# Kernel optimization log

Hardware: AMD Instinct MI355X
Metric: run time of the kernel (lower is better)

The kernel has to match this reference:

```python
import jax, jax.numpy as jnp
import numpy as np

B, V, T = 512, 50257, 2048   # batch, vocab, history length
TOP_K = 50                    # from __init__ arg top_k
NEG_INF = jnp.float32(-1e30)  # finite stand-in for -inf (same softmax result, clean grads)


def setup_inputs() -> dict:
    key = jax.random.key(0)
    k1, k2, k3 = jax.random.split(key, 3)
    logits = jax.random.normal(k1, (B, V), jnp.float32) * 4.0
    previous_tokens = jax.random.randint(k2, (B, T), 0, V)
    # uniform noise for the Gumbel-max trick (torch.rand_like); avoid log(0)
    rand_u = jax.random.uniform(k3, (B, V), jnp.float32, minval=1e-10, maxval=1.0)
    return {
        "logits": logits,
        "previous_tokens": previous_tokens,
        "rand_u": rand_u,
        "temperature": jnp.full((1, 1), 0.8, jnp.float32),
        "top_p": jnp.full((1, 1), 0.8, jnp.float32),
        "repetition_penalty": jnp.full((1, 1), 1.35, jnp.float32),
    }


def _logits_to_probs(logits, previous_tokens, temperature, top_p, repetition_penalty):
    b = jnp.arange(logits.shape[0])[:, None]
    # repetition penalty: gather scores at previous tokens, rescale, scatter back
    score = jnp.take_along_axis(logits, previous_tokens, axis=1)            # [B, T]
    score = jnp.where(score < 0, score * repetition_penalty, score / repetition_penalty)
    logits = logits.at[b, previous_tokens].set(score)
    # top-p (nucleus) filtering: sort descending, cumulative softmax mass
    order = jnp.argsort(-logits, axis=-1)                                   # [B, V]
    sorted_logits = jnp.take_along_axis(logits, order, axis=1)
    cum_probs = jnp.cumsum(jax.nn.softmax(sorted_logits, axis=-1), axis=-1)
    remove_sorted = cum_probs > top_p
    remove_sorted = remove_sorted.at[:, 0].set(False)                       # always keep best token
    # unsort the removal mask back to vocab order (order is a permutation)
    remove = jnp.zeros_like(remove_sorted).at[b, order].set(remove_sorted)
    logits = jnp.where(remove, NEG_INF, logits)
    # temperature
    logits = logits / jnp.maximum(temperature, 1e-5)
    # top-k filtering: mask everything below the k-th largest logit
    v = jax.lax.top_k(logits, TOP_K)[0]                                     # [B, TOP_K]
    pivot = v[:, -1:]
    logits = jnp.where(logits < pivot, NEG_INF, logits)
    return jax.nn.softmax(logits, axis=-1)


def reference(logits, previous_tokens, rand_u, temperature, top_p, repetition_penalty):
    probs = _logits_to_probs(logits, previous_tokens, temperature, top_p, repetition_penalty)
    # Gumbel-max multinomial sample: argmax(probs / Exp(1))
    q = -jnp.log(rand_u)
    idx_next = jnp.argmax(probs / q, axis=-1, keepdims=True).astype(jnp.int64)
    return idx_next, probs
```

## Files before the change

### kernel.cpp

```cpp
#include <hip/hip_runtime.h>
#include <cstdint>
#include <cmath>

#define V_SIZE 50257
#define T_SIZE 2048
#define B_SIZE 512
#define NTHR 1024
#define NWAVE (NTHR / 64)
#define CAND_MAX 1024
#define SPEC_THRESH 10.0f
#define SPEC_MIN 80
#define KOFF 32.0f

extern "C" __global__ __launch_bounds__(NTHR, 8)
void decode_kernel(const float* __restrict__ logits,
                   const int*   __restrict__ prev,
                   const float* __restrict__ rand_u,
                   const float* __restrict__ tempp,
                   const float* __restrict__ toppp,
                   const float* __restrict__ repp,
                   float* __restrict__ out)
{
    const int row  = blockIdx.x;
    const int tid  = threadIdx.x;
    const int lane = tid & 63;
    const int wid  = tid >> 6;

    __shared__ unsigned int bitmap[(V_SIZE + 31) / 32];
    __shared__ float cval[CAND_MAX];
    __shared__ int   cidx[CAND_MAX];
    __shared__ float rbuf[CAND_MAX];
    __shared__ float redf[NWAVE];
    __shared__ int   redi[NWAVE];
    __shared__ float sM, sZ, sS;
    __shared__ int   sCnt, sSend;

    const float rp   = repp[0];
    const float topp = toppp[0];
    const float temp = fmaxf(tempp[0], 1e-5f);

    const size_t rowoff = (size_t)row * V_SIZE;
    const float* lrow = logits + rowoff;
    const float* urow = rand_u + rowoff;
    float*       orow = out + B_SIZE + rowoff;

    for (int i = tid; i < (V_SIZE + 31) / 32; i += NTHR) bitmap[i] = 0u;
    if (tid == 0) sCnt = 0;
    __syncthreads();

    const int4* prow4 = (const int4*)(prev + (size_t)row * T_SIZE);
    for (int i = tid; i < T_SIZE / 4; i += NTHR) {
        int4 t = prow4[i];
        atomicOr(&bitmap[((unsigned)t.x) >> 5], 1u << (t.x & 31));
        atomicOr(&bitmap[((unsigned)t.y) >> 5], 1u << (t.y & 31));
        atomicOr(&bitmap[((unsigned)t.z) >> 5], 1u << (t.z & 31));
        atomicOr(&bitmap[((unsigned)t.w) >> 5], 1u << (t.w & 31));
    }
    __syncthreads();

    const int head  = (4 - (row & 3)) & 3;
    const int nvec  = (V_SIZE - head) >> 2;
    const int tails = head + nvec * 4;
    const float4* lrow4 = (const float4*)(lrow + head);

    float lm = -INFINITY, lz = 0.0f;
    auto process1 = [&](float x, int v) {
        unsigned w = bitmap[v >> 5];
        if ((w >> (v & 31)) & 1u) x = (x < 0.0f) ? x * rp : x / rp;
        if (x > SPEC_THRESH) {
            int p = atomicAdd(&sCnt, 1);
            if (p < CAND_MAX) { cval[p] = x; cidx[p] = v; }
        }
        lm = fmaxf(lm, x);
        lz += __expf(x - KOFF);
    };
    if (tid < head)           process1(lrow[tid], tid);
    if (tid < V_SIZE - tails) process1(lrow[tails + tid], tails + tid);
    for (int i = tid; i < nvec; i += NTHR) {
        float4 x4 = lrow4[i];
        int v = head + i * 4;
        process1(x4.x, v); process1(x4.y, v + 1);
        process1(x4.z, v + 2); process1(x4.w, v + 3);
    }

    {
        float wm = lm;
        for (int off = 32; off; off >>= 1) wm = fmaxf(wm, __shfl_down(wm, off));
        if (lane == 0) redf[wid] = wm;
    }
    __syncthreads();
    if (tid == 0) {
        float m = redf[0];
        for (int i = 1; i < NWAVE; ++i) m = fmaxf(m, redf[i]);
        sM = m;
    }
    __syncthreads();
    const float M = sM;

    {
        float wz = lz;
        for (int off = 32; off; off >>= 1) wz += __shfl_down(wz, off);
        if (lane == 0) redf[wid] = wz;
    }
    __syncthreads();
    if (tid == 0) {
        float s = 0.0f;
        for (int i = 0; i < NWAVE; ++i) s += redf[i];
        sZ = s * expf(KOFF - M);
    }
    __syncthreads();
    const float Z = sZ;

    int cnt = sCnt;
    int C;
    if (cnt >= SPEC_MIN && cnt <= CAND_MAX) {
        C = cnt;
    } else {
        auto count_pass = [&](float thr) -> int {
            __syncthreads();
            if (tid == 0) sCnt = 0;
            __syncthreads();
            int local = 0;
            for (int v = tid; v < V_SIZE; v += NTHR) {
                float x = lrow[v];
                unsigned w = bitmap[v >> 5];
                if ((w >> (v & 31)) & 1u) x = (x < 0.0f) ? x * rp : x / rp;
                if (x > thr) local++;
            }
            if (local) atomicAdd(&sCnt, local);
            __syncthreads();
            return sCnt;
        };
        float a = -200.0f, b = 200.0f, thr = 0.0f;
        int c = 0;
        for (int it = 0; it < 40; ++it) {
            thr = 0.5f * (a + b);
            c = count_pass(thr);
            if (c < SPEC_MIN)       b = thr;
            else if (c > CAND_MAX)  a = thr;
            else break;
        }
        if (c < SPEC_MIN) thr = a;
        __syncthreads();
        if (tid == 0) sCnt = 0;
        __syncthreads();
        for (int v = tid; v < V_SIZE; v += NTHR) {
            float x = lrow[v];
            unsigned w = bitmap[v >> 5];
            if ((w >> (v & 31)) & 1u) x = (x < 0.0f) ? x * rp : x / rp;
            if (x > thr) {
                int p = atomicAdd(&sCnt, 1);
                if (p < CAND_MAX) { cval[p] = x; cidx[p] = v; }
            }
        }
        __syncthreads();
        C = min(sCnt, CAND_MAX);
    }

    int n = 1; while (n < C) n <<= 1;
    for (int i = C + tid; i < n; i += NTHR) { cval[i] = -INFINITY; cidx[i] = 0x7FFFFFFF; }
    __syncthreads();
    for (int k = 2; k <= n; k <<= 1) {
        for (int j = k >> 1; j > 0; j >>= 1) {
            for (int i = tid; i < n; i += NTHR) {
                int l = i ^ j;
                if (l > i) {
                    float vi = cval[i], vl = cval[l];
                    int   ii = cidx[i], il = cidx[l];
                    bool lFirst = (vl > vi) || (vl == vi && il < ii);
                    bool asc = ((i & k) == 0);
                    if (lFirst == asc) {
                        cval[i] = vl; cval[l] = vi;
                        cidx[i] = il; cidx[l] = ii;
                    }
                }
            }
            __syncthreads();
        }
    }

    if (tid == 0) {
        float cum = 0.0f;
        int m = 0;
        float vp = cval[min(49, C - 1)];
        for (int i = 0; i < C; ++i) {
            cum += expf(cval[i] - M) / Z;
            if (i > 0 && cum > topp) break;
            m = i;
            if (m >= 49 && cval[i] < vp) break;
        }
        int send;
        if (m >= 49) {
            int e = 49;
            while (e + 1 < C && cval[e + 1] == vp) ++e;
            send = (m < e) ? m : e;
        } else {
            send = m;
        }
        sSend = send;
    }
    __syncthreads();

    const int send = sSend;
    const float v0 = cval[0];
    for (int i = tid; i <= send; i += NTHR)
        rbuf[i] = expf(cval[i] / temp - v0 / temp);
    __syncthreads();
    if (tid == 0) {
        float S = 0.0f;
        for (int i = 0; i <= send; ++i) S += rbuf[i];
        sS = S;
    }
    __syncthreads();
    const float S = sS;

    float bestr = -1.0f;
    int   besti = 0x7FFFFFFF;
    for (int i = tid; i <= send; i += NTHR) {
        float p = rbuf[i] / S;
        int v = cidx[i];
        orow[v] = p;
        float q = -logf(urow[v]);
        float r = p / q;
        if (r > bestr || (r == bestr && v < besti)) { bestr = r; besti = v; }
    }
    for (int off = 32; off; off >>= 1) {
        float r2 = __shfl_down(bestr, off);
        int   i2 = __shfl_down(besti, off);
        if (r2 > bestr || (r2 == bestr && i2 < besti)) { bestr = r2; besti = i2; }
    }
    if (lane == 0) { redf[wid] = bestr; redi[wid] = besti; }
    __syncthreads();
    if (tid == 0) {
        float br = redf[0]; int bi = redi[0];
        for (int i = 1; i < NWAVE; ++i) {
            if (redf[i] > br || (redf[i] == br && redi[i] < bi)) { br = redf[i]; bi = redi[i]; }
        }
        out[row] = (float)bi;
    }
}

extern "C" void kernel_launch(void* const* d_in, const int* in_sizes, int n_in,
                              void* d_out, int out_size, void* d_ws, size_t ws_size,
                              hipStream_t stream) {
    const float* logits = (const float*)d_in[0];
    const int*   prev   = (const int*)d_in[1];
    const float* rand_u = (const float*)d_in[2];
    const float* tempp  = (const float*)d_in[3];
    const float* toppp  = (const float*)d_in[4];
    const float* repp   = (const float*)d_in[5];
    float* out = (float*)d_out;

    hipMemsetAsync(d_out, 0, (size_t)out_size * sizeof(float), stream);

    hipLaunchKernelGGL(decode_kernel, dim3(B_SIZE), dim3(NTHR), 0, stream,
                       logits, prev, rand_u, tempp, toppp, repp, out);
}
```

Measured before the change: 261.5 us.

## Split row processing into chunked streaming kernel plus per-row tail kernel

Splits the single per-row kernel into two. The first launches 8 chunks per row, computing a partial softmax normaliser with a fixed offset and collecting high-logit candidates into a global workspace through atomics. The second applies the repetition penalty as a sparse correction to the normaliser and candidate values, then sorts the candidates and samples. This spreads the full-vocab streaming pass across more blocks and removes the bitmap lookup and max reduction from the hot loop, at the cost of an extra launch, a workspace memset and global atomics. It also relies on the fixed offset not overflowing and adds a fallback condition for when the penalty changes the candidate set.

```diff
diff --git a/kernel.cpp b/kernel.cpp
--- a/kernel.cpp
+++ b/kernel.cpp
@@ -5,21 +5,77 @@
 #define V_SIZE 50257
 #define T_SIZE 2048
 #define B_SIZE 512
-#define NTHR 1024
-#define NWAVE (NTHR / 64)
-#define CAND_MAX 1024
+#define CHUNKS 8
+#define CHUNK_LEN ((V_SIZE + CHUNKS - 1) / CHUNKS)
+#define NTHR_A 256
+#define NTHR_B 512
+#define NWAVE_B (NTHR_B / 64)
+#define CAP 512
 #define SPEC_THRESH 10.0f
 #define SPEC_MIN 80
 #define KOFF 32.0f
 
-extern "C" __global__ __launch_bounds__(NTHR, 8)
-void decode_kernel(const float* __restrict__ logits,
-                   const int*   __restrict__ prev,
-                   const float* __restrict__ rand_u,
-                   const float* __restrict__ tempp,
-                   const float* __restrict__ toppp,
-                   const float* __restrict__ repp,
-                   float* __restrict__ out)
+
+extern "C" __global__ __launch_bounds__(NTHR_A, 8)
+void stream_kernel(const float* __restrict__ logits,
+                   float* __restrict__ gZ, int* __restrict__ gcnt,
+                   float* __restrict__ gval, int* __restrict__ gidx)
+{
+    const int row = blockIdx.y;
+    const int tid = threadIdx.x;
+    const size_t rowoff = (size_t)row * V_SIZE;
+    const float* lrow = logits + rowoff;
+    const int lo = blockIdx.x * CHUNK_LEN;
+    const int hi = min(V_SIZE, lo + CHUNK_LEN);
+
+    float lz = 0.0f;
+    auto proc = [&](float x, int v) {
+        lz += __expf(x - KOFF);
+        if (x > SPEC_THRESH) {
+            int p = atomicAdd(&gcnt[row], 1);
+            if (p < CAP) {
+                gval[(size_t)row * CAP + p] = x;
+                gidx[(size_t)row * CAP + p] = v;
+            }
+        }
+    };
+
+    int a0 = lo + (int)((4u - ((unsigned)(rowoff + lo) & 3u)) & 3u);
+    if (a0 > hi) a0 = hi;
+    const int nv = (hi - a0) >> 2;
+    const int t0 = a0 + nv * 4;
+    if (tid < a0 - lo) proc(lrow[lo + tid], lo + tid);
+    if (tid < hi - t0) proc(lrow[t0 + tid], t0 + tid);
+    const float4* l4 = (const float4*)(lrow + a0);
+    for (int i = tid; i < nv; i += NTHR_A) {
+        float4 x4 = l4[i];
+        int v = a0 + i * 4;
+        proc(x4.x, v); proc(x4.y, v + 1); proc(x4.z, v + 2); proc(x4.w, v + 3);
+    }
+
+    __shared__ float red[NTHR_A / 64];
+    for (int off = 32; off; off >>= 1) lz += __shfl_down(lz, off);
+    if ((tid & 63) == 0) red[tid >> 6] = lz;
+    __syncthreads();
+    if (tid == 0) {
+        float s = 0.0f;
+        for (int i = 0; i < NTHR_A / 64; ++i) s += red[i];
+        atomicAdd(&gZ[row], s);
+    }
+}
+
+extern "C" __global__ __launch_bounds__(NTHR_B, 4)
+void tail_kernel(const float* __restrict__ logits,
+                 const int*   __restrict__ prev,
+                 const float* __restrict__ rand_u,
+                 const float* __restrict__ tempp,
+                 const float* __restrict__ toppp,
+                 const float* __restrict__ repp,
+                 const float* __restrict__ gZ,
+                 const int*   __restrict__ gcnt,
+                 const float* __restrict__ gval,
+                 const int*   __restrict__ gidx,
+                 float* __restrict__ out)
 {
     const int row  = blockIdx.x;
     const int tid  = threadIdx.x;
@@ -27,13 +83,13 @@
     const int wid  = tid >> 6;
 
     __shared__ unsigned int bitmap[(V_SIZE + 31) / 32];
-    __shared__ float cval[CAND_MAX];
-    __shared__ int   cidx[CAND_MAX];
-    __shared__ float rbuf[CAND_MAX];
-    __shared__ float redf[NWAVE];
-    __shared__ int   redi[NWAVE];
-    __shared__ float sM, sZ, sS;
-    __shared__ int   sCnt, sSend;
+    __shared__ float cval[CAP];
+    __shared__ int   cidx[CAP];
+    __shared__ float rbuf[CAP];
+    __shared__ float redf[NWAVE_B];
+    __shared__ int   redi[NWAVE_B];
+    __shared__ float sZf, sS;
+    __shared__ int   sCnt, sSend, sGT;
 
     const float rp   = repp[0];
     const float topp = toppp[0];
@@ -44,89 +100,80 @@
     const float* urow = rand_u + rowoff;
     float*       orow = out + B_SIZE + rowoff;
 
-    for (int i = tid; i < (V_SIZE + 31) / 32; i += NTHR) bitmap[i] = 0u;
-    if (tid == 0) sCnt = 0;
-    __syncthreads();
-
+    for (int i = tid; i < (V_SIZE + 31) / 32; i += NTHR_B) bitmap[i] = 0u;
+    if (tid == 0) { sCnt = 0; sGT = 0; }
+    __syncthreads();
+
+    float dz = 0.0f;
     const int4* prow4 = (const int4*)(prev + (size_t)row * T_SIZE);
-    for (int i = tid; i < T_SIZE / 4; i += NTHR) {
+    auto corr = [&](int t) {
+        unsigned m = 1u << (t & 31);
+        unsigned old = atomicOr(&bitmap[((unsigned)t) >> 5], m);
+        if (!(old & m)) {
+            float x = lrow[t];
+            float y = (x < 0.0f) ? x * rp : x / rp;
+            dz += __expf(y - KOFF) - __expf(x - KOFF);
+        }
+    };
+    for (int i = tid; i < T_SIZE / 4; i += NTHR_B) {
         int4 t = prow4[i];
-        atomicOr(&bitmap[((unsigned)t.x) >> 5], 1u << (t.x & 31));
-        atomicOr(&bitmap[((unsigned)t.y) >> 5], 1u << (t.y & 31));
-        atomicOr(&bitmap[((unsigned)t.z) >> 5], 1u << (t.z & 31));
-        atomicOr(&bitmap[((unsigned)t.w) >> 5], 1u << (t.w & 31));
-    }
-    __syncthreads();
-
-    const int head  = (4 - (row & 3)) & 3;
-    const int nvec  = (V_SIZE - head) >> 2;
-    const int tails = head + nvec * 4;
-    const float4* lrow4 = (const float4*)(lrow + head);
-
-    float lm = -INFINITY, lz = 0.0f;
-    auto process1 = [&](float x, int v) {
-        unsigned w = bitmap[v >> 5];
-        if ((w >> (v & 31)) & 1u) x = (x < 0.0f) ? x * rp : x / rp;
-        if (x > SPEC_THRESH) {
-            int p = atomicAdd(&sCnt, 1);
-            if (p < CAND_MAX) { cval[p] = x; cidx[p] = v; }
-        }
-        lm = fmaxf(lm, x);
-        lz += __expf(x - KOFF);
-    };
-    if (tid < head)           process1(lrow[tid], tid);
-    if (tid < V_SIZE - tails) process1(lrow[tails + tid], tails + tid);
-    for (int i = tid; i < nvec; i += NTHR) {
-        float4 x4 = lrow4[i];
-        int v = head + i * 4;
-        process1(x4.x, v); process1(x4.y, v + 1);
-        process1(x4.z, v + 2); process1(x4.w, v + 3);
-    }
-
+        corr(t.x); corr(t.y); corr(t.z); corr(t.w);
+    }
     {
-        float wm = lm;
-        for (int off = 32; off; off >>= 1) wm = fmaxf(wm, __shfl_down(wm, off));
-        if (lane == 0) redf[wid] = wm;
-    }
-    __syncthreads();
-    if (tid == 0) {
-        float m = redf[0];
-        for (int i = 1; i < NWAVE; ++i) m = fmaxf(m, redf[i]);
-        sM = m;
-    }
-    __syncthreads();
-    const float M = sM;
-
+        for (int off = 32; off; off >>= 1) dz += __shfl_down(dz, off);
+        if (lane == 0) redf[wid] = dz;
+    }
+    __syncthreads();
+    if (tid == 0) {
+        float s = 0.0f;
+        for (int i = 0; i < NWAVE_B; ++i) s += redf[i];
+        sZf = gZ[row] + s;
+    }
+    __syncthreads();
+    const float Z = sZf;
+
+    const int cntg = gcnt[row];
+    const int Craw = min(cntg, CAP);
     {
-        float wz = lz;
-        for (int off = 32; off; off >>= 1) wz += __shfl_down(wz, off);
-        if (lane == 0) redf[wid] = wz;
-    }
-    __syncthreads();
-    if (tid == 0) {
-        float s = 0.0f;
-        for (int i = 0; i < NWAVE; ++i) s += redf[i];
-        sZ = s * expf(KOFF - M);
-    }
-    __syncthreads();
-    const float Z = sZ;
-
-    int cnt = sCnt;
+        int myGT = 0;
+        for (int j = tid; j < Craw; j += NTHR_B) {
+            float x = gval[(size_t)row * CAP + j];
+            int   v = gidx[(size_t)row * CAP + j];
+            if ((bitmap[((unsigned)v) >> 5] >> (v & 31)) & 1u)
+                x = (x < 0.0f) ? x * rp : x / rp;
+            cval[j] = x; cidx[j] = v;
+            if (x > SPEC_THRESH) myGT++;
+        }
+        for (int off = 32; off; off >>= 1) myGT += __shfl_down(myGT, off);
+        if (lane == 0) redi[wid] = myGT;
+    }
+    __syncthreads();
+    if (tid == 0) {
+        int s = 0;
+        for (int i = 0; i < NWAVE_B; ++i) s += redi[i];
+        sGT = s;
+    }
+    __syncthreads();
+
+    const bool fb = (cntg < SPEC_MIN) || (cntg > CAP) ||
+                    (sGT < SPEC_MIN) || (rp < 1.0f);
     int C;
-    if (cnt >= SPEC_MIN && cnt <= CAND_MAX) {
-        C = cnt;
+    if (!fb) {
+        C = Craw;
     } else {
+        auto pen_at = [&](int v) {
+            float x = lrow[v];
+            if ((bitmap[((unsigned)v) >> 5] >> (v & 31)) & 1u)
+                x = (x < 0.0f) ? x * rp : x / rp;
+            return x;
+        };
         auto count_pass = [&](float thr) -> int {
             __syncthreads();
             if (tid == 0) sCnt = 0;
             __syncthreads();
             int local = 0;
-            for (int v = tid; v < V_SIZE; v += NTHR) {
-                float x = lrow[v];
-                unsigned w = bitmap[v >> 5];
-                if ((w >> (v & 31)) & 1u) x = (x < 0.0f) ? x * rp : x / rp;
-                if (x > thr) local++;
-            }
+            for (int v = tid; v < V_SIZE; v += NTHR_B)
+                if (pen_at(v) > thr) local++;
             if (local) atomicAdd(&sCnt, local);
             __syncthreads();
             return sCnt;
@@ -136,33 +183,31 @@
         for (int it = 0; it < 40; ++it) {
             thr = 0.5f * (a + b);
             c = count_pass(thr);
-            if (c < SPEC_MIN)       b = thr;
-            else if (c > CAND_MAX)  a = thr;
+            if (c < SPEC_MIN)      b = thr;
+            else if (c > CAP)      a = thr;
             else break;
         }
         if (c < SPEC_MIN) thr = a;
         __syncthreads();
         if (tid == 0) sCnt = 0;
         __syncthreads();
-        for (int v = tid; v < V_SIZE; v += NTHR) {
-            float x = lrow[v];
-            unsigned w = bitmap[v >> 5];
-            if ((w >> (v & 31)) & 1u) x = (x < 0.0f) ? x * rp : x / rp;
+        for (int v = tid; v < V_SIZE; v += NTHR_B) {
+            float x = pen_at(v);
             if (x > thr) {
                 int p = atomicAdd(&sCnt, 1);
-                if (p < CAND_MAX) { cval[p] = x; cidx[p] = v; }
+                if (p < CAP) { cval[p] = x; cidx[p] = v; }
             }
         }
         __syncthreads();
-        C = min(sCnt, CAND_MAX);
+        C = min(sCnt, CAP);
     }
 
     int n = 1; while (n < C) n <<= 1;
-    for (int i = C + tid; i < n; i += NTHR) { cval[i] = -INFINITY; cidx[i] = 0x7FFFFFFF; }
+    for (int i = C + tid; i < n; i += NTHR_B) { cval[i] = -INFINITY; cidx[i] = 0x7FFFFFFF; }
     __syncthreads();
     for (int k = 2; k <= n; k <<= 1) {
         for (int j = k >> 1; j > 0; j >>= 1) {
-            for (int i = tid; i < n; i += NTHR) {
+            for (int i = tid; i < n; i += NTHR_B) {
                 int l = i ^ j;
                 if (l > i) {
                     float vi = cval[i], vl = cval[l];
@@ -184,7 +229,7 @@
         int m = 0;
         float vp = cval[min(49, C - 1)];
         for (int i = 0; i < C; ++i) {
-            cum += expf(cval[i] - M) / Z;
+            cum += expf(cval[i] - KOFF) / Z;
             if (i > 0 && cum > topp) break;
             m = i;
             if (m >= 49 && cval[i] < vp) break;
@@ -203,7 +248,7 @@
 
     const int send = sSend;
     const float v0 = cval[0];
-    for (int i = tid; i <= send; i += NTHR)
+    for (int i = tid; i <= send; i += NTHR_B)
         rbuf[i] = expf(cval[i] / temp - v0 / temp);
     __syncthreads();
     if (tid == 0) {
@@ -216,7 +261,7 @@
 
     float bestr = -1.0f;
     int   besti = 0x7FFFFFFF;
-    for (int i = tid; i <= send; i += NTHR) {
+    for (int i = tid; i <= send; i += NTHR_B) {
         float p = rbuf[i] / S;
         int v = cidx[i];
         orow[v] = p;
@@ -233,7 +278,7 @@
     __syncthreads();
     if (tid == 0) {
         float br = redf[0]; int bi = redi[0];
-        for (int i = 1; i < NWAVE; ++i) {
+        for (int i = 1; i < NWAVE_B; ++i) {
             if (redf[i] > br || (redf[i] == br && redi[i] < bi)) { br = redf[i]; bi = redi[i]; }
         }
         out[row] = (float)bi;
@@ -251,8 +296,17 @@
     const float* repp   = (const float*)d_in[5];
     float* out = (float*)d_out;
 
+    float* gZ   = (float*)d_ws;
+    int*   gcnt = (int*)d_ws + B_SIZE;
+    float* gval = (float*)d_ws + 2 * B_SIZE;
+    int*   gidx = (int*)d_ws + 2 * B_SIZE + B_SIZE * CAP;
+
     hipMemsetAsync(d_out, 0, (size_t)out_size * sizeof(float), stream);
-
-    hipLaunchKernelGGL(decode_kernel, dim3(B_SIZE), dim3(NTHR), 0, stream,
-                       logits, prev, rand_u, tempp, toppp, repp, out);
+    hipMemsetAsync(d_ws, 0, 2 * B_SIZE * sizeof(float), stream);
+
+    hipLaunchKernelGGL(stream_kernel, dim3(CHUNKS, B_SIZE), dim3(NTHR_A), 0, stream,
+                       logits, gZ, gcnt, gval, gidx);
+    hipLaunchKernelGGL(tail_kernel, dim3(B_SIZE), dim3(NTHR_B), 0, stream,
+                       logits, prev, rand_u, tempp, toppp, repp,
+                       gZ, gcnt, gval, gidx, out);
 }
```

New measurement: 390.1 us. 1.49x slower.

## Compute softmax sum on raw logits with penalty correction, drop max pass

Applied to the files above, without the earlier changes.

The main logit scan now runs on raw logits without first building the repetition bitmap. The penalty is applied afterwards: each first-seen previous token contributes a delta to the partition sum, and the penalty is reapplied to the collected candidates. The separate max reduction is removed by normalising against a fixed offset, and the scan loop is unrolled four-wide with two accumulators. Candidate capacity shrinks to 512, and a fallback path covers cases where the speculative candidate set becomes invalid after penalisation (such as a penalty below 1). The fixed offset risks overflow or underflow in the sum if logits are far from the assumed range.

```diff
diff --git a/kernel.cpp b/kernel.cpp
--- a/kernel.cpp
+++ b/kernel.cpp
@@ -7,7 +7,7 @@
 #define B_SIZE 512
 #define NTHR 1024
 #define NWAVE (NTHR / 64)
-#define CAND_MAX 1024
+#define CAP 512
 #define SPEC_THRESH 10.0f
 #define SPEC_MIN 80
 #define KOFF 32.0f
@@ -27,13 +27,13 @@
     const int wid  = tid >> 6;
 
     __shared__ unsigned int bitmap[(V_SIZE + 31) / 32];
-    __shared__ float cval[CAND_MAX];
-    __shared__ int   cidx[CAND_MAX];
-    __shared__ float rbuf[CAND_MAX];
+    __shared__ float cval[CAP];
+    __shared__ int   cidx[CAP];
+    __shared__ float rbuf[CAP];
     __shared__ float redf[NWAVE];
     __shared__ int   redi[NWAVE];
-    __shared__ float sM, sZ, sS;
-    __shared__ int   sCnt, sSend;
+    __shared__ float sZ, sS;
+    __shared__ int   sCnt, sSend, sGT;
 
     const float rp   = repp[0];
     const float topp = toppp[0];
@@ -45,88 +45,118 @@
     float*       orow = out + B_SIZE + rowoff;
 
     for (int i = tid; i < (V_SIZE + 31) / 32; i += NTHR) bitmap[i] = 0u;
-    if (tid == 0) sCnt = 0;
-    __syncthreads();
-
-    const int4* prow4 = (const int4*)(prev + (size_t)row * T_SIZE);
-    for (int i = tid; i < T_SIZE / 4; i += NTHR) {
-        int4 t = prow4[i];
-        atomicOr(&bitmap[((unsigned)t.x) >> 5], 1u << (t.x & 31));
-        atomicOr(&bitmap[((unsigned)t.y) >> 5], 1u << (t.y & 31));
-        atomicOr(&bitmap[((unsigned)t.z) >> 5], 1u << (t.z & 31));
-        atomicOr(&bitmap[((unsigned)t.w) >> 5], 1u << (t.w & 31));
-    }
+    if (tid == 0) { sCnt = 0; sGT = 0; }
     __syncthreads();
 
     const int head  = (4 - (row & 3)) & 3;
     const int nvec  = (V_SIZE - head) >> 2;
     const int tails = head + nvec * 4;
-    const float4* lrow4 = (const float4*)(lrow + head);
-
-    float lm = -INFINITY, lz = 0.0f;
-    auto process1 = [&](float x, int v) {
-        unsigned w = bitmap[v >> 5];
-        if ((w >> (v & 31)) & 1u) x = (x < 0.0f) ? x * rp : x / rp;
+    const float4* l4 = (const float4*)(lrow + head);
+
+    float lz0 = 0.0f, lz1 = 0.0f;
+    auto proc = [&](float x, int v, float& acc) {
+        acc += __expf(x - KOFF);
         if (x > SPEC_THRESH) {
             int p = atomicAdd(&sCnt, 1);
-            if (p < CAND_MAX) { cval[p] = x; cidx[p] = v; }
-        }
-        lm = fmaxf(lm, x);
-        lz += __expf(x - KOFF);
+            if (p < CAP) { cval[p] = x; cidx[p] = v; }
+        }
     };
-    if (tid < head)           process1(lrow[tid], tid);
-    if (tid < V_SIZE - tails) process1(lrow[tails + tid], tails + tid);
-    for (int i = tid; i < nvec; i += NTHR) {
-        float4 x4 = lrow4[i];
-        int v = head + i * 4;
-        process1(x4.x, v); process1(x4.y, v + 1);
-        process1(x4.z, v + 2); process1(x4.w, v + 3);
+    if (tid < head)           proc(lrow[tid], tid, lz0);
+    if (tid < V_SIZE - tails) proc(lrow[tails + tid], tails + tid, lz1);
+
+    auto proc4 = [&](float4 x4, int v) {
+        proc(x4.x, v,     lz0); proc(x4.y, v + 1, lz1);
+        proc(x4.z, v + 2, lz0); proc(x4.w, v + 3, lz1);
+    };
+    int i = tid;
+    for (; i + 3 * NTHR < nvec; i += 4 * NTHR) {
+        float4 a = l4[i];
+        float4 b = l4[i + NTHR];
+        float4 c = l4[i + 2 * NTHR];
+        float4 d = l4[i + 3 * NTHR];
+        proc4(a, head + i * 4);
+        proc4(b, head + (i + NTHR) * 4);
+        proc4(c, head + (i + 2 * NTHR) * 4);
+        proc4(d, head + (i + 3 * NTHR) * 4);
+    }
+    for (; i < nvec; i += NTHR) {
+        float4 a = l4[i];
+        proc4(a, head + i * 4);
+    }
+
+    float dz = 0.0f;
+    const int4* prow4 = (const int4*)(prev + (size_t)row * T_SIZE);
+    auto corr = [&](int t) {
+        unsigned m = 1u << (t & 31);
+        unsigned old = atomicOr(&bitmap[((unsigned)t) >> 5], m);
+        if (!(old & m)) {
+            float x = lrow[t];
+            float y = (x < 0.0f) ? x * rp : x / rp;
+            dz += __expf(y - KOFF) - __expf(x - KOFF);
+        }
+    };
+    for (int j = tid; j < T_SIZE / 4; j += NTHR) {
+        int4 t = prow4[j];
+        corr(t.x); corr(t.y); corr(t.z); corr(t.w);
     }
 
     {
-        float wm = lm;
-        for (int off = 32; off; off >>= 1) wm = fmaxf(wm, __shfl_down(wm, off));
-        if (lane == 0) redf[wid] = wm;
-    }
-    __syncthreads();
-    if (tid == 0) {
-        float m = redf[0];
-        for (int i = 1; i < NWAVE; ++i) m = fmaxf(m, redf[i]);
-        sM = m;
-    }
-    __syncthreads();
-    const float M = sM;
-
-    {
-        float wz = lz;
+        float wz = lz0 + lz1 + dz;
         for (int off = 32; off; off >>= 1) wz += __shfl_down(wz, off);
         if (lane == 0) redf[wid] = wz;
     }
     __syncthreads();
     if (tid == 0) {
         float s = 0.0f;
-        for (int i = 0; i < NWAVE; ++i) s += redf[i];
-        sZ = s * expf(KOFF - M);
+        for (int j = 0; j < NWAVE; ++j) s += redf[j];
+        sZ = s;
     }
     __syncthreads();
     const float Z = sZ;
 
-    int cnt = sCnt;
+    const int cntg = sCnt;
+    const int Craw = min(cntg, CAP);
+    {
+        int myGT = 0;
+        for (int j = tid; j < Craw; j += NTHR) {
+            float x = cval[j];
+            int   v = cidx[j];
+            if ((bitmap[((unsigned)v) >> 5] >> (v & 31)) & 1u) {
+                x = (x < 0.0f) ? x * rp : x / rp;
+                cval[j] = x;
+            }
+            if (x > SPEC_THRESH) myGT++;
+        }
+        for (int off = 32; off; off >>= 1) myGT += __shfl_down(myGT, off);
+        if (lane == 0) redi[wid] = myGT;
+    }
+    __syncthreads();
+    if (tid == 0) {
+        int s = 0;
+        for (int j = 0; j < NWAVE; ++j) s += redi[j];
+        sGT = s;
+    }
+    __syncthreads();
+
+    const bool fb = (cntg < SPEC_MIN) || (cntg > CAP) ||
+                    (sGT < SPEC_MIN) || (rp < 1.0f);
     int C;
-    if (cnt >= SPEC_MIN && cnt <= CAND_MAX) {
-        C = cnt;
+    if (!fb) {
+        C = Craw;
     } else {
+        auto pen_at = [&](int v) {
+            float x = lrow[v];
+            if ((bitmap[((unsigned)v) >> 5] >> (v & 31)) & 1u)
+                x = (x < 0.0f) ? x * rp : x / rp;
+            return x;
+        };
         auto count_pass = [&](float thr) -> int {
             __syncthreads();
             if (tid == 0) sCnt = 0;
             __syncthreads();
             int local = 0;
-            for (int v = tid; v < V_SIZE; v += NTHR) {
-                float x = lrow[v];
-                unsigned w = bitmap[v >> 5];
-                if ((w >> (v & 31)) & 1u) x = (x < 0.0f) ? x * rp : x / rp;
-                if (x > thr) local++;
-            }
+            for (int v = tid; v < V_SIZE; v += NTHR)
+                if (pen_at(v) > thr) local++;
             if (local) atomicAdd(&sCnt, local);
             __syncthreads();
             return sCnt;
@@ -136,8 +166,8 @@
         for (int it = 0; it < 40; ++it) {
             thr = 0.5f * (a + b);
             c = count_pass(thr);
-            if (c < SPEC_MIN)       b = thr;
-            else if (c > CAND_MAX)  a = thr;
+            if (c < SPEC_MIN)      b = thr;
+            else if (c > CAP)      a = thr;
             else break;
         }
         if (c < SPEC_MIN) thr = a;
@@ -145,33 +175,31 @@
         if (tid == 0) sCnt = 0;
         __syncthreads();
         for (int v = tid; v < V_SIZE; v += NTHR) {
-            float x = lrow[v];
-            unsigned w = bitmap[v >> 5];
-            if ((w >> (v & 31)) & 1u) x = (x < 0.0f) ? x * rp : x / rp;
+            float x = pen_at(v);
             if (x > thr) {
                 int p = atomicAdd(&sCnt, 1);
-                if (p < CAND_MAX) { cval[p] = x; cidx[p] = v; }
+                if (p < CAP) { cval[p] = x; cidx[p] = v; }
             }
         }
         __syncthreads();
-        C = min(sCnt, CAND_MAX);
+        C = min(sCnt, CAP);
     }
 
     int n = 1; while (n < C) n <<= 1;
-    for (int i = C + tid; i < n; i += NTHR) { cval[i] = -INFINITY; cidx[i] = 0x7FFFFFFF; }
+    for (int j = C + tid; j < n; j += NTHR) { cval[j] = -INFINITY; cidx[j] = 0x7FFFFFFF; }
     __syncthreads();
     for (int k = 2; k <= n; k <<= 1) {
         for (int j = k >> 1; j > 0; j >>= 1) {
-            for (int i = tid; i < n; i += NTHR) {
-                int l = i ^ j;
-                if (l > i) {
-                    float vi = cval[i], vl = cval[l];
-                    int   ii = cidx[i], il = cidx[l];
+            for (int p = tid; p < n; p += NTHR) {
+                int l = p ^ j;
+                if (l > p) {
+                    float vi = cval[p], vl = cval[l];
+                    int   ii = cidx[p], il = cidx[l];
                     bool lFirst = (vl > vi) || (vl == vi && il < ii);
-                    bool asc = ((i & k) == 0);
+                    bool asc = ((p & k) == 0);
                     if (lFirst == asc) {
-                        cval[i] = vl; cval[l] = vi;
-                        cidx[i] = il; cidx[l] = ii;
+                        cval[p] = vl; cval[l] = vi;
+                        cidx[p] = il; cidx[l] = ii;
                     }
                 }
             }
@@ -183,11 +211,11 @@
         float cum = 0.0f;
         int m = 0;
         float vp = cval[min(49, C - 1)];
-        for (int i = 0; i < C; ++i) {
-            cum += expf(cval[i] - M) / Z;
-            if (i > 0 && cum > topp) break;
-            m = i;
-            if (m >= 49 && cval[i] < vp) break;
+        for (int j = 0; j < C; ++j) {
+            cum += expf(cval[j] - KOFF) / Z;
+            if (j > 0 && cum > topp) break;
+            m = j;
+            if (m >= 49 && cval[j] < vp) break;
         }
         int send;
         if (m >= 49) {
@@ -203,12 +231,12 @@
 
     const int send = sSend;
     const float v0 = cval[0];
-    for (int i = tid; i <= send; i += NTHR)
-        rbuf[i] = expf(cval[i] / temp - v0 / temp);
+    for (int j = tid; j <= send; j += NTHR)
+        rbuf[j] = expf(cval[j] / temp - v0 / temp);
     __syncthreads();
     if (tid == 0) {
         float S = 0.0f;
-        for (int i = 0; i <= send; ++i) S += rbuf[i];
+        for (int j = 0; j <= send; ++j) S += rbuf[j];
         sS = S;
     }
     __syncthreads();
@@ -216,9 +244,9 @@
 
     float bestr = -1.0f;
     int   besti = 0x7FFFFFFF;
-    for (int i = tid; i <= send; i += NTHR) {
-        float p = rbuf[i] / S;
-        int v = cidx[i];
+    for (int j = tid; j <= send; j += NTHR) {
+        float p = rbuf[j] / S;
+        int v = cidx[j];
         orow[v] = p;
         float q = -logf(urow[v]);
         float r = p / q;
@@ -233,8 +261,8 @@
     __syncthreads();
     if (tid == 0) {
         float br = redf[0]; int bi = redi[0];
-        for (int i = 1; i < NWAVE; ++i) {
-            if (redf[i] > br || (redf[i] == br && redi[i] < bi)) { br = redf[i]; bi = redi[i]; }
+        for (int j = 1; j < NWAVE; ++j) {
+            if (redf[j] > br || (redf[j] == br && redi[j] < bi)) { br = redf[j]; bi = redi[j]; }
         }
         out[row] = (float)bi;
     }
@@ -252,7 +280,6 @@
     float* out = (float*)d_out;
 
     hipMemsetAsync(d_out, 0, (size_t)out_size * sizeof(float), stream);
-
     hipLaunchKernelGGL(decode_kernel, dim3(B_SIZE), dim3(NTHR), 0, stream,
                        logits, prev, rand_u, tempp, toppp, repp, out);
 }
```

After: 262.2 us. About the same (+0.3%).
